# Performance work log

Hardware: AMD Instinct MI355X
Metric: run time of the kernel (lower is better)

Reference implementation:

```python
import jax, jax.numpy as jnp
import numpy as np

DIM = 256; Hh = 64; Ww = 64; L = Hh * Ww; B = 2
DIN = DIM          # expand = 1
DST = 16           # d_state
DTR = 16           # dt_rank = ceil(dim/16)
DCONV = 4


def _ln(x, g, b, eps=1e-5):
    m = jnp.mean(x, -1, keepdims=True)
    v = jnp.mean((x - m) ** 2, -1, keepdims=True)
    return (x - m) / jnp.sqrt(v + eps) * g + b


def _scan_dir(x, ep, z, convW, convb, xpW, dtW, dtb, A_log, Dp):
    # x, ep, z: (B, d_inner, L)
    xc = jnp.pad(x, ((0, 0), (0, 0), (DCONV - 1, 0)))  # causal depthwise conv
    xc = jax.lax.conv_general_dilated(
        xc, convW[:, None, :], (1,), 'VALID',
        feature_group_count=DIN, dimension_numbers=('NCH', 'OIH', 'NCH'))
    xs = jax.nn.silu(xc + convb[None, :, None])
    # cross: dt, B, C come from the OTHER modality's embedding (v7 cross-SSM)
    xdbl = jnp.einsum('bdl,kd->bkl', ep, xpW)               # (B, DTR+2N, L)
    dt = jax.nn.softplus(jnp.einsum('brl,dr->bdl', xdbl[:, :DTR], dtW) + dtb[None, :, None])
    Bm = xdbl[:, DTR:DTR + DST]                             # (B, N, L)
    Cm = xdbl[:, DTR + DST:]                                # (B, N, L)
    A = -jnp.exp(A_log)                                     # (d, N)
    dA = jnp.exp(jnp.einsum('bdl,dn->bdln', dt, A))         # (B, d, L, N)
    dBx = jnp.einsum('bdl,bnl,bdl->bdln', dt, Bm, xs)
    def comb(c1, c2):
        a1, b1 = c1; a2, b2 = c2
        return a1 * a2, a2 * b1 + b2
    _, h = jax.lax.associative_scan(comb, (dA, dBx), axis=2)  # h_l = dA_l h_{l-1} + dBx_l
    y = jnp.einsum('bdln,bnl->bdl', h, Cm) + Dp[None, :, None] * xs
    return y * jax.nn.silu(z)


def _mamba(u, e, in_proj_W, extra_proj_W,
           convf_W, convf_b, xprojf_W, dtf_W, dtf_b, A_log_f, D_f,
           convb_W, convb_b, xprojb_W, dtb_W, dtb_b, A_log_b, D_b,
           outnorm_g, outnorm_b, out_proj_W):
    xz = u @ in_proj_W.T                                    # (B, L, 2*d_inner)
    x = xz[..., :DIN].transpose(0, 2, 1)                    # (B, d, L)
    z = xz[..., DIN:].transpose(0, 2, 1)
    ep = (e @ extra_proj_W.T).transpose(0, 2, 1)            # (B, d, L)
    yf = _scan_dir(x, ep, z, convf_W, convf_b, xprojf_W, dtf_W, dtf_b, A_log_f, D_f)
    yb = jnp.flip(_scan_dir(jnp.flip(x, -1), jnp.flip(ep, -1), jnp.flip(z, -1),
                            convb_W, convb_b, xprojb_W, dtb_W, dtb_b, A_log_b, D_b), -1)
    y = (yf + yb) * 0.5                                     # if_devide_out
    y = _ln(y.transpose(0, 2, 1), outnorm_g, outnorm_b)     # use_norm
    return y @ out_proj_W.T


def setup_inputs() -> dict:
    key = jax.random.key(0)
    ks = jax.random.split(key, 20)
    s = 0.05
    dt_bias = float(np.log(np.expm1(0.01)))
    inp = {
        'input0': jax.random.normal(ks[0], (B, L, DIM), jnp.float32),
        'input1': jax.random.normal(ks[1], (B, L, DIM), jnp.float32),
        'norm0_g': jnp.ones((DIM,), jnp.float32), 'norm0_b': jnp.zeros((DIM,), jnp.float32),
        'norm1_g': jnp.ones((DIM,), jnp.float32), 'norm1_b': jnp.zeros((DIM,), jnp.float32),
        'cw_W': jax.random.normal(ks[2], (DIM, 2 * DIM), jnp.float32) * s,
        'cw_b': jnp.zeros((DIM,), jnp.float32),
        'in_proj_W': jax.random.normal(ks[3], (2 * DIN, DIM), jnp.float32) * s,
        'extra_proj_W': jax.random.normal(ks[4], (DIN, DIM), jnp.float32) * s,
        'convf_W': jax.random.normal(ks[5], (DIN, DCONV), jnp.float32) * 0.3,
        'convf_b': jnp.zeros((DIN,), jnp.float32),
        'xprojf_W': jax.random.normal(ks[6], (DTR + 2 * DST, DIN), jnp.float32) * s,
        'dtf_W': jax.random.normal(ks[7], (DIN, DTR), jnp.float32) * s,
        'dtf_b': jnp.full((DIN,), dt_bias, jnp.float32),
        'A_log_f': jnp.broadcast_to(jnp.log(jnp.arange(1, DST + 1, dtype=jnp.float32)), (DIN, DST)).copy(),
        'D_f': jnp.ones((DIN,), jnp.float32),
        'convb_W': jax.random.normal(ks[8], (DIN, DCONV), jnp.float32) * 0.3,
        'convb_b': jnp.zeros((DIN,), jnp.float32),
        'xprojb_W': jax.random.normal(ks[9], (DTR + 2 * DST, DIN), jnp.float32) * s,
        'dtb_W': jax.random.normal(ks[10], (DIN, DTR), jnp.float32) * s,
        'dtb_b': jnp.full((DIN,), dt_bias, jnp.float32),
        'A_log_b': jnp.broadcast_to(jnp.log(jnp.arange(1, DST + 1, dtype=jnp.float32)), (DIN, DST)).copy(),
        'D_b': jnp.ones((DIN,), jnp.float32),
        'outnorm_g': jnp.ones((DIN,), jnp.float32), 'outnorm_b': jnp.zeros((DIN,), jnp.float32),
        'out_proj_W': jax.random.normal(ks[11], (DIM, DIN), jnp.float32) * s,
        'post_g': jnp.ones((DIM,), jnp.float32), 'post_b': jnp.zeros((DIM,), jnp.float32),
    }
    return inp


def reference(input0, input1, norm0_g, norm0_b, norm1_g, norm1_b, cw_W, cw_b,
              in_proj_W, extra_proj_W,
              convf_W, convf_b, xprojf_W, dtf_W, dtf_b, A_log_f, D_f,
              convb_W, convb_b, xprojb_W, dtb_W, dtb_b, A_log_b, D_b,
              outnorm_g, outnorm_b, out_proj_W, post_g, post_b):
    skip = input0
    x0 = _ln(input0, norm0_g, norm0_b)
    x1 = _ln(input1, norm1_g, norm1_b)
    w = jax.nn.sigmoid(jnp.concatenate([x0, x1], -1) @ cw_W.T + cw_b)
    out = _mamba(x0, x1, in_proj_W, extra_proj_W,
                 convf_W, convf_b, xprojf_W, dtf_W, dtf_b, A_log_f, D_f,
                 convb_W, convb_b, xprojb_W, dtb_W, dtb_b, A_log_b, D_b,
                 outnorm_g, outnorm_b, out_proj_W)
    out = _ln(out, post_g, post_b)
    out = out * w + x0 * (1 - w)
    return out + skip
```

## Files before the change

### kernel.cpp

```cpp
#include <hip/hip_runtime.h>
#include <cstddef>

#define LL 4096
#define BB 2
#define DD 256
#define NEL ((size_t)BB * LL * DD)

typedef __bf16 bf16x8 __attribute__((ext_vector_type(8)));
typedef float f32x4 __attribute__((ext_vector_type(4)));
typedef unsigned short u16;

__device__ __forceinline__ float4 ld4(const float* p) { return *reinterpret_cast<const float4*>(p); }
__device__ __forceinline__ void st4(float* p, const float4 v) { *reinterpret_cast<float4*>(p) = v; }
__device__ __forceinline__ float softplusf(float x) { return fmaxf(x, 0.f) + log1pf(expf(-fabsf(x))); }
__device__ __forceinline__ u16 f2b(float f) {
    union { float f; unsigned u; } v; v.f = f;
    unsigned u = v.u;
    return (u16)((u + 0x7fffu + ((u >> 16) & 1u)) >> 16);
}

__device__ __forceinline__ void load16(const float* __restrict__ p, int fwd, float* dst) {
    if (fwd) {
#pragma unroll
        for (int k = 0; k < 4; ++k) {
            float4 v = ld4(p + 4 * k);
            dst[4 * k] = v.x; dst[4 * k + 1] = v.y; dst[4 * k + 2] = v.z; dst[4 * k + 3] = v.w;
        }
    } else {
#pragma unroll
        for (int k = 0; k < 4; ++k) {
            float4 v = ld4(p + 4 * k);
            dst[15 - 4 * k] = v.x; dst[14 - 4 * k] = v.y; dst[13 - 4 * k] = v.z; dst[12 - 4 * k] = v.w;
        }
    }
}


__global__ __launch_bounds__(256) void prep_q(
    const float* __restrict__ xpf, const float* __restrict__ xpb,
    const float* __restrict__ extW, float* __restrict__ Q, u16* __restrict__ wsH)
{
    const int r = blockIdx.x % 48;
    const int dir = blockIdx.x / 48;
    const int k = threadIdx.x;
    const float* xp = dir ? xpb : xpf;
    float s = 0.f;
    for (int n = 0; n < 256; ++n) s = fmaf(xp[r * 256 + n], extW[n * 256 + k], s);
    if (r < 16) Q[(dir * 16 + r) * 256 + k] = s;
    else        wsH[393216 + ((dir ? 32 : 0) + (r - 16)) * 256 + k] = f2b(s);
}

__global__ __launch_bounds__(256) void prep_w(
    const float* __restrict__ inW, const float* __restrict__ cwW,
    const float* __restrict__ outW, const float* __restrict__ dtfW,
    const float* __restrict__ dtbW, const float* __restrict__ Q,
    u16* __restrict__ wsH)
{
    const int idx = blockIdx.x * 256 + threadIdx.x;
    if (idx < 131072) {
        wsH[idx] = f2b(inW[idx]);
    } else if (idx < 262144) {
        wsH[idx] = f2b(cwW[idx - 131072]);
    } else if (idx < 393216) {
        const int i = idx - 262144;
        const int dir = i >> 16;
        const int j = i & 65535;
        const int n = j >> 8, k = j & 255;
        const float* dtW = dir ? dtbW : dtfW;
        const float* Qd = Q + dir * 4096;
        float s = 0.f;
#pragma unroll
        for (int r = 0; r < 16; ++r) s = fmaf(dtW[n * 16 + r], Qd[r * 256 + k], s);
        wsH[idx] = f2b(s);
    } else if (idx >= 409600 && idx < 475136) {
        wsH[idx] = f2b(outW[idx - 409600]);
    }
}

__global__ __launch_bounds__(64) void ln_rows(
    const float* __restrict__ in, float* __restrict__ outf, u16* __restrict__ outh,
    const float* __restrict__ g, const float* __restrict__ bb)
{
    const int row = blockIdx.x;
    const int t = threadIdx.x;
    const size_t off = (size_t)row * 256 + t * 4;
    float4 v = ld4(&in[off]);
    float s = v.x + v.y + v.z + v.w;
    float s2 = v.x * v.x + v.y * v.y + v.z * v.z + v.w * v.w;
#pragma unroll
    for (int dl = 1; dl < 64; dl <<= 1) { s += __shfl_xor(s, dl); s2 += __shfl_xor(s2, dl); }
    const float m = s * (1.f / 256.f);
    const float var = s2 * (1.f / 256.f) - m * m;
    const float rstd = rsqrtf(var + 1e-5f);
    const float4 gv = ld4(&g[t * 4]);
    const float4 bv = ld4(&bb[t * 4]);
    float4 r;
    r.x = (v.x - m) * rstd * gv.x + bv.x;
    r.y = (v.y - m) * rstd * gv.y + bv.y;
    r.z = (v.z - m) * rstd * gv.z + bv.z;
    r.w = (v.w - m) * rstd * gv.w + bv.w;
    if (outf) st4(&outf[off], r);
    ushort4 h; h.x = f2b(r.x); h.y = f2b(r.y); h.z = f2b(r.z); h.w = f2b(r.w);
    *reinterpret_cast<ushort4*>(&outh[off]) = h;
}

__global__ __launch_bounds__(256) void gemm_mfma(
    const u16* __restrict__ x0h, const u16* __restrict__ x1h, const u16* __restrict__ wsH,
    const float* __restrict__ cwb, const float* __restrict__ dtfb, const float* __restrict__ dtbb,
    float* __restrict__ xT, float* __restrict__ zT, float* __restrict__ wbuf,
    float* __restrict__ dtfT, float* __restrict__ dtbT,
    float* __restrict__ bcfT, float* __restrict__ bcbT)
{
    __shared__ __align__(16) u16 Blds[64 * 256];
    const int t = threadIdx.x;
    const int lane = t & 63;
    const int wid = t >> 6;
    const int col = lane & 15;
    const int kq = lane >> 4;
    const int m0 = blockIdx.x * 128;
    const int by = blockIdx.y;

    int seg, nbase, ldk, nhalf; const u16* W;
    if (by < 4)       { seg = 0; W = wsH + (size_t)(by * 64) * 256;                 ldk = 256; nhalf = 1; nbase = by * 64; }
    else if (by < 8)  { seg = 1; W = wsH + (size_t)(by * 64) * 256;                 ldk = 256; nhalf = 1; nbase = (by - 4) * 64; }
    else if (by < 12) { seg = 2; W = wsH + 131072 + (size_t)((by - 8) * 64) * 512;  ldk = 512; nhalf = 2; nbase = (by - 8) * 64; }
    else if (by < 16) { seg = 3; W = wsH + 262144 + (size_t)((by - 12) * 64) * 256; ldk = 256; nhalf = 1; nbase = (by - 12) * 64; }
    else if (by < 20) { seg = 4; W = wsH + 327680 + (size_t)((by - 16) * 64) * 256; ldk = 256; nhalf = 1; nbase = (by - 16) * 64; }
    else              { seg = 5; W = wsH + 393216;                                  ldk = 256; nhalf = 1; nbase = 0; }

    const u16* A0 = (seg >= 3) ? x1h : x0h;
    const int arow = m0 + wid * 32 + col;

    f32x4 acc[2][4] = {};
    for (int half = 0; half < nhalf; ++half) {
        if (half) __syncthreads();
#pragma unroll
        for (int it = 0; it < 8; ++it) {
            const int c = it * 256 + t;
            const int row = c >> 5, kc = c & 31;
            const bf16x8 v = *reinterpret_cast<const bf16x8*>(W + (size_t)row * ldk + half * 256 + kc * 8);
            const unsigned byt = ((unsigned)(row * 512 + kc * 16)) ^ (((unsigned)row & 7u) << 4);
            *reinterpret_cast<bf16x8*>(reinterpret_cast<char*>(Blds) + byt) = v;
        }
        __syncthreads();
        const u16* Ap = (seg == 2 && half) ? x1h : A0;
        const u16* Abase = Ap + (size_t)arow * 256;
        for (int k0 = 0; k0 < 256; k0 += 32) {
            const int kk = k0 + kq * 8;
            const bf16x8 a0 = *reinterpret_cast<const bf16x8*>(Abase + kk);
            const bf16x8 a1 = *reinterpret_cast<const bf16x8*>(Abase + 16 * 256 + kk);
#pragma unroll
            for (int nf = 0; nf < 4; ++nf) {
                const int n = nf * 16 + col;
                const unsigned byt = ((unsigned)(n * 512 + k0 * 2 + kq * 16)) ^ (((unsigned)n & 7u) << 4);
                const bf16x8 bfr = *reinterpret_cast<const bf16x8*>(reinterpret_cast<const char*>(Blds) + byt);
                acc[0][nf] = __builtin_amdgcn_mfma_f32_16x16x32_bf16(a0, bfr, acc[0][nf], 0, 0, 0);
                acc[1][nf] = __builtin_amdgcn_mfma_f32_16x16x32_bf16(a1, bfr, acc[1][nf], 0, 0, 0);
            }
        }
    }

    const int bb2 = m0 >> 12;
    const int l0 = m0 & (LL - 1);

    if (seg == 0 || seg == 1) {
        float* dst = (seg == 0) ? xT : zT;
#pragma unroll
        for (int rg = 0; rg < 2; ++rg) {
            const int mrow = wid * 32 + rg * 16 + kq * 4;
#pragma unroll
            for (int nf = 0; nf < 4; ++nf) {
                const int d = nbase + nf * 16 + col;
                *reinterpret_cast<f32x4*>(&dst[((size_t)bb2 * DD + d) * LL + l0 + mrow]) = acc[rg][nf];
            }
        }
    } else if (seg == 2) {
#pragma unroll
        for (int rg = 0; rg < 2; ++rg) {
            const int mrow = wid * 32 + rg * 16 + kq * 4;
#pragma unroll
            for (int nf = 0; nf < 4; ++nf) {
                const int n = nbase + nf * 16 + col;
                const float bv = cwb[n];
#pragma unroll
                for (int r = 0; r < 4; ++r)
                    wbuf[(size_t)(m0 + mrow + r) * 256 + n] = 1.f / (1.f + expf(-(acc[rg][nf][r] + bv)));
            }
        }
    } else if (seg == 3 || seg == 4) {
        const float* bias = (seg == 3) ? dtfb : dtbb;
        float* dst = (seg == 3) ? dtfT : dtbT;
#pragma unroll
        for (int rg = 0; rg < 2; ++rg) {
            const int mrow = wid * 32 + rg * 16 + kq * 4;
#pragma unroll
            for (int nf = 0; nf < 4; ++nf) {
                const int d = nbase + nf * 16 + col;
                const float bv = bias[d];
                f32x4 o;
#pragma unroll
                for (int r = 0; r < 4; ++r) o[r] = softplusf(acc[rg][nf][r] + bv);
                *reinterpret_cast<f32x4*>(&dst[((size_t)bb2 * DD + d) * LL + l0 + mrow]) = o;
            }
        }
    } else {
#pragma unroll
        for (int rg = 0; rg < 2; ++rg) {
            const int mrow = wid * 32 + rg * 16 + kq * 4;
#pragma unroll
            for (int nf = 0; nf < 4; ++nf) {
                const int n = nf * 16 + col;
                float* dst = (n < 32) ? bcfT : bcbT;
                const int comp = n & 31;
                *reinterpret_cast<f32x4*>(&dst[((size_t)bb2 * 32 + comp) * LL + l0 + mrow]) = acc[rg][nf];
            }
        }
    }
}

__global__ __launch_bounds__(256) void gemm_out_mfma(
    const u16* __restrict__ ynh, const u16* __restrict__ wsH, float* __restrict__ out)
{
    __shared__ __align__(16) u16 Blds[64 * 256];
    const int t = threadIdx.x;
    const int lane = t & 63;
    const int wid = t >> 6;
    const int col = lane & 15;
    const int kq = lane >> 4;
    const int m0 = blockIdx.x * 128;
    const int n0 = blockIdx.y * 64;
    const u16* W = wsH + 409600 + (size_t)n0 * 256;
    const int arow = m0 + wid * 32 + col;

#pragma unroll
    for (int it = 0; it < 8; ++it) {
        const int c = it * 256 + t;
        const int row = c >> 5, kc = c & 31;
        const bf16x8 v = *reinterpret_cast<const bf16x8*>(W + (size_t)row * 256 + kc * 8);
        const unsigned byt = ((unsigned)(row * 512 + kc * 16)) ^ (((unsigned)row & 7u) << 4);
        *reinterpret_cast<bf16x8*>(reinterpret_cast<char*>(Blds) + byt) = v;
    }
    __syncthreads();

    f32x4 acc[2][4] = {};
    const u16* Abase = ynh + (size_t)arow * 256;
    for (int k0 = 0; k0 < 256; k0 += 32) {
        const int kk = k0 + kq * 8;
        const bf16x8 a0 = *reinterpret_cast<const bf16x8*>(Abase + kk);
        const bf16x8 a1 = *reinterpret_cast<const bf16x8*>(Abase + 16 * 256 + kk);
#pragma unroll
        for (int nf = 0; nf < 4; ++nf) {
            const int n = nf * 16 + col;
            const unsigned byt = ((unsigned)(n * 512 + k0 * 2 + kq * 16)) ^ (((unsigned)n & 7u) << 4);
            const bf16x8 bfr = *reinterpret_cast<const bf16x8*>(reinterpret_cast<const char*>(Blds) + byt);
            acc[0][nf] = __builtin_amdgcn_mfma_f32_16x16x32_bf16(a0, bfr, acc[0][nf], 0, 0, 0);
            acc[1][nf] = __builtin_amdgcn_mfma_f32_16x16x32_bf16(a1, bfr, acc[1][nf], 0, 0, 0);
        }
    }
#pragma unroll
    for (int rg = 0; rg < 2; ++rg) {
        const int mrow = wid * 32 + rg * 16 + kq * 4;
#pragma unroll
        for (int nf = 0; nf < 4; ++nf) {
            const int n = n0 + nf * 16 + col;
#pragma unroll
            for (int r = 0; r < 4; ++r)
                out[(size_t)(m0 + mrow + r) * 256 + n] = acc[rg][nf][r];
        }
    }
}

__global__ __launch_bounds__(256) void scan_kernel(
    const float* __restrict__ xT, const float* __restrict__ zT,
    const float* __restrict__ dtfT, const float* __restrict__ dtbT,
    const float* __restrict__ bcfT, const float* __restrict__ bcbT,
    const float* __restrict__ cfW, const float* __restrict__ cfB,
    const float* __restrict__ cbW, const float* __restrict__ cbB,
    const float* __restrict__ AlF, const float* __restrict__ AlB,
    const float* __restrict__ DF, const float* __restrict__ DB,
    float* __restrict__ yF, float* __restrict__ yB)
{
    const int d = blockIdx.x;
    const int b = blockIdx.y;
    const int dir = blockIdx.z;
    const int t = threadIdx.x;
    const int lane = t & 63;
    const int wv = t >> 6;
    const int fwd = (dir == 0);
    const float* dtT = fwd ? dtfT : dtbT;
    const float* bcT = fwd ? bcfT : bcbT;
    const float* cW  = fwd ? cfW  : cbW;
    const float* cBv = fwd ? cfB  : cbB;
    const float* Al  = fwd ? AlF  : AlB;
    const float* Dp  = fwd ? DF   : DB;
    float* yout = fwd ? yF : yB;

    const int p0 = t * 16;
    const size_t xbase = ((size_t)b * DD + d) * LL;
    const int ls = LL - 16 - p0;
    const int off16 = fwd ? p0 : ls;

    const float Dd = Dp[d];
    const float c0 = cW[d * 4 + 0], c1 = cW[d * 4 + 1], c2 = cW[d * 4 + 2], c3 = cW[d * 4 + 3];
    const float cbias = cBv[d];

    float xq[19];
    if (fwd) {
#pragma unroll
        for (int k = 0; k < 4; ++k) {
            float4 v = ld4(&xT[xbase + p0 + 4 * k]);
            xq[3 + 4 * k] = v.x; xq[4 + 4 * k] = v.y; xq[5 + 4 * k] = v.z; xq[6 + 4 * k] = v.w;
        }
        xq[2] = (p0 >= 1) ? xT[xbase + p0 - 1] : 0.f;
        xq[1] = (p0 >= 2) ? xT[xbase + p0 - 2] : 0.f;
        xq[0] = (p0 >= 3) ? xT[xbase + p0 - 3] : 0.f;
    } else {
#pragma unroll
        for (int k = 0; k < 4; ++k) {
            float4 v = ld4(&xT[xbase + ls + 4 * k]);
            xq[18 - 4 * k] = v.x; xq[17 - 4 * k] = v.y; xq[16 - 4 * k] = v.z; xq[15 - 4 * k] = v.w;
        }
        xq[2] = (p0 >= 1) ? xT[xbase + LL - p0] : 0.f;
        xq[1] = (p0 >= 2) ? xT[xbase + LL + 1 - p0] : 0.f;
        xq[0] = (p0 >= 3) ? xT[xbase + LL + 2 - p0] : 0.f;
    }

    float dt[16];
    load16(&dtT[xbase + off16], fwd, dt);

    float dtxs[16], yacc[16];
#pragma unroll
    for (int s = 0; s < 16; ++s) {
        float c = fmaf(xq[s], c0, fmaf(xq[s + 1], c1, fmaf(xq[s + 2], c2, fmaf(xq[s + 3], c3, cbias))));
        const float xv = c / (1.f + expf(-c));
        dtxs[s] = dt[s] * xv;
        yacc[s] = Dd * xv;
    }

    const float* bcb0 = bcT + (size_t)b * 32 * LL + off16;

    __shared__ float wPs[2][4];
    __shared__ float wSs[2][4];

#pragma unroll 1
    for (int n = 0; n < 16; ++n) {
        const float a2 = -expf(Al[d * 16 + n]) * 1.4426950408889634f;
        float Bn[16];
        load16(bcb0 + (size_t)n * LL, fwd, Bn);
        float pw[16], hl[16];
        float Pl = 1.f, Sl = 0.f;
#pragma unroll
        for (int s = 0; s < 16; ++s) {
            const float w = exp2f(dt[s] * a2);
            Sl = fmaf(w, Sl, dtxs[s] * Bn[s]);
            Pl *= w;
            pw[s] = Pl; hl[s] = Sl;
        }
        float Cn[16];
        load16(bcb0 + (size_t)(16 + n) * LL, fwd, Cn);
#pragma unroll
        for (int dl = 1; dl < 64; dl <<= 1) {
            const float Pp = __shfl_up(Pl, dl);
            const float Sp = __shfl_up(Sl, dl);
            if (lane >= dl) { Sl = fmaf(Pl, Sp, Sl); Pl *= Pp; }
        }
        const int buf = n & 1;
        if (lane == 63) { wPs[buf][wv] = Pl; wSs[buf][wv] = Sl; }
        __syncthreads();
        float WSv = 0.f;
#pragma unroll
        for (int w2 = 0; w2 < 3; ++w2)
            if (w2 < wv) WSv = fmaf(wPs[buf][w2], WSv, wSs[buf][w2]);
        const float Pex = __shfl_up(Pl, 1);
        const float Sex = __shfl_up(Sl, 1);
        const float hin = lane ? fmaf(Pex, WSv, Sex) : WSv;
#pragma unroll
        for (int s = 0; s < 16; ++s)
            yacc[s] = fmaf(fmaf(pw[s], hin, hl[s]), Cn[s], yacc[s]);
    }

    float zq[16];
    load16(&zT[xbase + off16], fwd, zq);
    float yv[16];
#pragma unroll
    for (int s = 0; s < 16; ++s) {
        const float zz = zq[s];
        yv[s] = yacc[s] * zz / (1.f + expf(-zz));
    }

    if (fwd) {
#pragma unroll
        for (int k = 0; k < 4; ++k)
            st4(&yout[xbase + p0 + 4 * k], make_float4(yv[4 * k], yv[4 * k + 1], yv[4 * k + 2], yv[4 * k + 3]));
    } else {
#pragma unroll
        for (int k = 0; k < 4; ++k)
            st4(&yout[xbase + ls + 4 * k], make_float4(yv[15 - 4 * k], yv[14 - 4 * k], yv[13 - 4 * k], yv[12 - 4 * k]));
    }
}

__global__ __launch_bounds__(256) void comb_ln(
    const float* __restrict__ yF, const float* __restrict__ yB,
    const float* __restrict__ g, const float* __restrict__ bb,
    u16* __restrict__ out)
{
    __shared__ float tile[256][33];
    __shared__ float rs[8][32];
    __shared__ float rs2[8][32];
    const int b = blockIdx.y;
    const int l0 = blockIdx.x * 32;
    const int t = threadIdx.x;
    {
        const size_t base = ((size_t)b * DD + t) * LL + l0;
#pragma unroll
        for (int k = 0; k < 8; ++k) {
            float4 f = ld4(&yF[base + 4 * k]);
            float4 bv = ld4(&yB[base + 4 * k]);
            tile[t][4 * k + 0] = (f.x + bv.x) * 0.5f;
            tile[t][4 * k + 1] = (f.y + bv.y) * 0.5f;
            tile[t][4 * k + 2] = (f.z + bv.z) * 0.5f;
            tile[t][4 * k + 3] = (f.w + bv.w) * 0.5f;
        }
    }
    __syncthreads();
    const int l = t & 31;
    const int grp = t >> 5;
    float s = 0.f, s2 = 0.f;
#pragma unroll
    for (int i = 0; i < 32; ++i) {
        const float v = tile[grp * 32 + i][l];
        s += v; s2 = fmaf(v, v, s2);
    }
    rs[grp][l] = s; rs2[grp][l] = s2;
    __syncthreads();
    float st = 0.f, st2 = 0.f;
#pragma unroll
    for (int gq = 0; gq < 8; ++gq) { st += rs[gq][l]; st2 += rs2[gq][l]; }
    const float m = st * (1.f / 256.f);
    const float var = st2 * (1.f / 256.f) - m * m;
    const float rstd = rsqrtf(var + 1e-5f);
    const size_t obase = ((size_t)b * LL + l0 + l) * 256 + grp * 32;
#pragma unroll
    for (int k = 0; k < 8; ++k) {
        const float4 gv = ld4(&g[grp * 32 + 4 * k]);
        const float4 bv2 = ld4(&bb[grp * 32 + 4 * k]);
        ushort4 h;
        h.x = f2b((tile[grp * 32 + 4 * k + 0][l] - m) * rstd * gv.x + bv2.x);
        h.y = f2b((tile[grp * 32 + 4 * k + 1][l] - m) * rstd * gv.y + bv2.y);
        h.z = f2b((tile[grp * 32 + 4 * k + 2][l] - m) * rstd * gv.z + bv2.z);
        h.w = f2b((tile[grp * 32 + 4 * k + 3][l] - m) * rstd * gv.w + bv2.w);
        *reinterpret_cast<ushort4*>(&out[obase + 4 * k]) = h;
    }
}

__global__ __launch_bounds__(64) void final_kernel(
    const float* __restrict__ o, const float* __restrict__ w,
    const float* __restrict__ x0n, const float* __restrict__ in0,
    const float* __restrict__ pg, const float* __restrict__ pb,
    float* __restrict__ outp)
{
    const int row = blockIdx.x;
    const int t = threadIdx.x;
    const size_t off = (size_t)row * 256 + t * 4;
    float4 v = ld4(&o[off]);
    float s = v.x + v.y + v.z + v.w;
    float s2 = v.x * v.x + v.y * v.y + v.z * v.z + v.w * v.w;
#pragma unroll
    for (int dl = 1; dl < 64; dl <<= 1) { s += __shfl_xor(s, dl); s2 += __shfl_xor(s2, dl); }
    const float m = s * (1.f / 256.f);
    const float var = s2 * (1.f / 256.f) - m * m;
    const float rstd = rsqrtf(var + 1e-5f);
    const float4 gv = ld4(&pg[t * 4]);
    const float4 bv = ld4(&pb[t * 4]);
    const float4 wv = ld4(&w[off]);
    const float4 xv = ld4(&x0n[off]);
    const float4 iv = ld4(&in0[off]);
    float4 r;
    r.x = ((v.x - m) * rstd * gv.x + bv.x) * wv.x + xv.x * (1.f - wv.x) + iv.x;
    r.y = ((v.y - m) * rstd * gv.y + bv.y) * wv.y + xv.y * (1.f - wv.y) + iv.y;
    r.z = ((v.z - m) * rstd * gv.z + bv.z) * wv.z + xv.z * (1.f - wv.z) + iv.z;
    r.w = ((v.w - m) * rstd * gv.w + bv.w) * wv.w + xv.w * (1.f - wv.w) + iv.w;
    st4(&outp[off], r);
}

extern "C" void kernel_launch(void* const* d_in, const int* in_sizes, int n_in,
                              void* d_out, int out_size, void* d_ws, size_t ws_size,
                              hipStream_t stream) {
    (void)in_sizes; (void)n_in; (void)out_size; (void)ws_size;
    const float* in0      = (const float*)d_in[0];
    const float* in1      = (const float*)d_in[1];
    const float* norm0_g  = (const float*)d_in[2];
    const float* norm0_b  = (const float*)d_in[3];
    const float* norm1_g  = (const float*)d_in[4];
    const float* norm1_b  = (const float*)d_in[5];
    const float* cw_W     = (const float*)d_in[6];
    const float* cw_b     = (const float*)d_in[7];
    const float* in_proj_W    = (const float*)d_in[8];
    const float* extra_proj_W = (const float*)d_in[9];
    const float* convf_W  = (const float*)d_in[10];
    const float* convf_b  = (const float*)d_in[11];
    const float* xprojf_W = (const float*)d_in[12];
    const float* dtf_W    = (const float*)d_in[13];
    const float* dtf_b    = (const float*)d_in[14];
    const float* A_log_f  = (const float*)d_in[15];
    const float* D_f      = (const float*)d_in[16];
    const float* convb_W  = (const float*)d_in[17];
    const float* convb_b  = (const float*)d_in[18];
    const float* xprojb_W = (const float*)d_in[19];
    const float* dtb_W    = (const float*)d_in[20];
    const float* dtb_b    = (const float*)d_in[21];
    const float* A_log_b  = (const float*)d_in[22];
    const float* D_b      = (const float*)d_in[23];
    const float* outnorm_g = (const float*)d_in[24];
    const float* outnorm_b = (const float*)d_in[25];
    const float* out_proj_W = (const float*)d_in[26];
    const float* post_g   = (const float*)d_in[27];
    const float* post_b   = (const float*)d_in[28];

    float* ws = (float*)d_ws;
    float* x0n   = ws;
    float* xT    = ws + NEL;
    float* zT    = ws + 2 * NEL;
    float* dtfT  = ws + 3 * NEL;
    float* dtbT  = ws + 4 * NEL;
    float* wbuf  = ws + 5 * NEL;
    float* yF    = ws + 6 * NEL;
    float* yB    = ws + 7 * NEL;
    float* bcfT  = ws + 8 * NEL;
    float* bcbT  = bcfT + (size_t)BB * 32 * LL;
    u16*   wsH   = (u16*)(bcbT + (size_t)BB * 32 * LL);
    float* Qtmp  = (float*)(wsH + 475136);

    u16* x0h = (u16*)yF;
    u16* x1h = x0h + NEL;
    u16* ynormh = (u16*)dtfT;
    float* obuf = dtbT;

    prep_q<<<96, 256, 0, stream>>>(xprojf_W, xprojb_W, extra_proj_W, Qtmp, wsH);
    prep_w<<<1856, 256, 0, stream>>>(in_proj_W, cw_W, out_proj_W, dtf_W, dtb_W, Qtmp, wsH);
    ln_rows<<<BB * LL, 64, 0, stream>>>(in0, x0n, x0h, norm0_g, norm0_b);
    ln_rows<<<BB * LL, 64, 0, stream>>>(in1, nullptr, x1h, norm1_g, norm1_b);
    gemm_mfma<<<dim3(64, 21, 1), 256, 0, stream>>>(x0h, x1h, wsH, cw_b, dtf_b, dtb_b,
                                                   xT, zT, wbuf, dtfT, dtbT, bcfT, bcbT);
    scan_kernel<<<dim3(256, 2, 2), 256, 0, stream>>>(xT, zT, dtfT, dtbT, bcfT, bcbT,
                                                     convf_W, convf_b, convb_W, convb_b,
                                                     A_log_f, A_log_b, D_f, D_b,
                                                     yF, yB);
    comb_ln<<<dim3(128, 2, 1), 256, 0, stream>>>(yF, yB, outnorm_g, outnorm_b, ynormh);
    gemm_out_mfma<<<dim3(64, 4, 1), 256, 0, stream>>>(ynormh, wsH, obuf);
    final_kernel<<<BB * LL, 64, 0, stream>>>(obuf, wbuf, x0n, in0, post_g, post_b, (float*)d_out);
}
```

Baseline: 132.7 us.

## Split scan state dimension across two blocks and store partial outputs as bf16

The scan kernel now launches twice as many blocks, with each block handling 8 of the 16 state channels and writing a partial output. The D*x term is added only in one half, and both partials are multiplied by silu(z). Partials are stored as bf16 and summed in comb_ln, which now reads four bf16 buffers. This is meant to add parallelism to the scan and cut output bytes. In exchange the conv, silu and z work is done twice, and rounding each partial to bf16 adds error.

```diff
diff --git a/kernel.cpp b/kernel.cpp
--- a/kernel.cpp
+++ b/kernel.cpp
@@ -17,6 +17,9 @@
     union { float f; unsigned u; } v; v.f = f;
     unsigned u = v.u;
     return (u16)((u + 0x7fffu + ((u >> 16) & 1u)) >> 16);
+}
+__device__ __forceinline__ float b2f(unsigned bits16) {
+    union { unsigned u; float f; } v; v.u = bits16 << 16; return v.f;
 }
 
 __device__ __forceinline__ void load16(const float* __restrict__ p, int fwd, float* dst) {
@@ -278,11 +281,12 @@
     const float* __restrict__ cbW, const float* __restrict__ cbB,
     const float* __restrict__ AlF, const float* __restrict__ AlB,
     const float* __restrict__ DF, const float* __restrict__ DB,
-    float* __restrict__ yF, float* __restrict__ yB)
+    u16* __restrict__ yFh, u16* __restrict__ yBh)
 {
     const int d = blockIdx.x;
     const int b = blockIdx.y;
-    const int dir = blockIdx.z;
+    const int dir = blockIdx.z >> 1;
+    const int half = blockIdx.z & 1;
     const int t = threadIdx.x;
     const int lane = t & 63;
     const int wv = t >> 6;
@@ -293,7 +297,7 @@
     const float* cBv = fwd ? cfB  : cbB;
     const float* Al  = fwd ? AlF  : AlB;
     const float* Dp  = fwd ? DF   : DB;
-    float* yout = fwd ? yF : yB;
+    u16* yout = (fwd ? yFh : yBh) + (size_t)half * NEL;
 
     const int p0 = t * 16;
     const size_t xbase = ((size_t)b * DD + d) * LL;
@@ -334,7 +338,7 @@
         float c = fmaf(xq[s], c0, fmaf(xq[s + 1], c1, fmaf(xq[s + 2], c2, fmaf(xq[s + 3], c3, cbias))));
         const float xv = c / (1.f + expf(-c));
         dtxs[s] = dt[s] * xv;
-        yacc[s] = Dd * xv;
+        yacc[s] = half ? (Dd * xv) : 0.f;
     }
 
     const float* bcb0 = bcT + (size_t)b * 32 * LL + off16;
@@ -343,10 +347,11 @@
     __shared__ float wSs[2][4];
 
 #pragma unroll 1
-    for (int n = 0; n < 16; ++n) {
-        const float a2 = -expf(Al[d * 16 + n]) * 1.4426950408889634f;
+    for (int n = 0; n < 8; ++n) {
+        const int ng = half * 8 + n;
+        const float a2 = -expf(Al[d * 16 + ng]) * 1.4426950408889634f;
         float Bn[16];
-        load16(bcb0 + (size_t)n * LL, fwd, Bn);
+        load16(bcb0 + (size_t)ng * LL, fwd, Bn);
         float pw[16], hl[16];
         float Pl = 1.f, Sl = 0.f;
 #pragma unroll
@@ -357,7 +362,7 @@
             pw[s] = Pl; hl[s] = Sl;
         }
         float Cn[16];
-        load16(bcb0 + (size_t)(16 + n) * LL, fwd, Cn);
+        load16(bcb0 + (size_t)(16 + ng) * LL, fwd, Cn);
 #pragma unroll
         for (int dl = 1; dl < 64; dl <<= 1) {
             const float Pp = __shfl_up(Pl, dl);
@@ -388,19 +393,26 @@
         yv[s] = yacc[s] * zz / (1.f + expf(-zz));
     }
 
-    if (fwd) {
-#pragma unroll
-        for (int k = 0; k < 4; ++k)
-            st4(&yout[xbase + p0 + 4 * k], make_float4(yv[4 * k], yv[4 * k + 1], yv[4 * k + 2], yv[4 * k + 3]));
-    } else {
-#pragma unroll
-        for (int k = 0; k < 4; ++k)
-            st4(&yout[xbase + ls + 4 * k], make_float4(yv[15 - 4 * k], yv[14 - 4 * k], yv[13 - 4 * k], yv[12 - 4 * k]));
+#pragma unroll
+    for (int g = 0; g < 2; ++g) {
+        uint4 U;
+        unsigned* up = reinterpret_cast<unsigned*>(&U);
+        if (fwd) {
+#pragma unroll
+            for (int j = 0; j < 4; ++j)
+                up[j] = (unsigned)f2b(yv[8 * g + 2 * j]) | ((unsigned)f2b(yv[8 * g + 2 * j + 1]) << 16);
+            *reinterpret_cast<uint4*>(&yout[xbase + p0 + 8 * g]) = U;
+        } else {
+#pragma unroll
+            for (int j = 0; j < 4; ++j)
+                up[j] = (unsigned)f2b(yv[15 - 8 * g - 2 * j]) | ((unsigned)f2b(yv[15 - 8 * g - 2 * j - 1]) << 16);
+            *reinterpret_cast<uint4*>(&yout[xbase + ls + 8 * g]) = U;
+        }
     }
 }
 
 __global__ __launch_bounds__(256) void comb_ln(
-    const float* __restrict__ yF, const float* __restrict__ yB,
+    const u16* __restrict__ yFh, const u16* __restrict__ yBh,
     const float* __restrict__ g, const float* __restrict__ bb,
     u16* __restrict__ out)
 {
@@ -411,15 +423,30 @@
     const int l0 = blockIdx.x * 32;
     const int t = threadIdx.x;
     {
-        const size_t base = ((size_t)b * DD + t) * LL + l0;
-#pragma unroll
-        for (int k = 0; k < 8; ++k) {
-            float4 f = ld4(&yF[base + 4 * k]);
-            float4 bv = ld4(&yB[base + 4 * k]);
-            tile[t][4 * k + 0] = (f.x + bv.x) * 0.5f;
-            tile[t][4 * k + 1] = (f.y + bv.y) * 0.5f;
-            tile[t][4 * k + 2] = (f.z + bv.z) * 0.5f;
-            tile[t][4 * k + 3] = (f.w + bv.w) * 0.5f;
+        const size_t rowoff = ((size_t)b * DD + t) * LL + l0;
+        const u16* s0 = yFh + rowoff;
+        const u16* s1 = yFh + NEL + rowoff;
+        const u16* s2 = yBh + rowoff;
+        const u16* s3 = yBh + NEL + rowoff;
+#pragma unroll
+        for (int k = 0; k < 4; ++k) {
+            const uint4 a = *reinterpret_cast<const uint4*>(s0 + 8 * k);
+            const uint4 c = *reinterpret_cast<const uint4*>(s1 + 8 * k);
+            const uint4 e = *reinterpret_cast<const uint4*>(s2 + 8 * k);
+            const uint4 f = *reinterpret_cast<const uint4*>(s3 + 8 * k);
+            const unsigned* au = reinterpret_cast<const unsigned*>(&a);
+            const unsigned* cu = reinterpret_cast<const unsigned*>(&c);
+            const unsigned* eu = reinterpret_cast<const unsigned*>(&e);
+            const unsigned* fu = reinterpret_cast<const unsigned*>(&f);
+#pragma unroll
+            for (int j = 0; j < 4; ++j) {
+                const float lo = b2f(au[j] & 0xffffu) + b2f(cu[j] & 0xffffu)
+                               + b2f(eu[j] & 0xffffu) + b2f(fu[j] & 0xffffu);
+                const float hi = b2f(au[j] >> 16) + b2f(cu[j] >> 16)
+                               + b2f(eu[j] >> 16) + b2f(fu[j] >> 16);
+                tile[t][8 * k + 2 * j]     = lo * 0.5f;
+                tile[t][8 * k + 2 * j + 1] = hi * 0.5f;
+            }
         }
     }
     __syncthreads();
@@ -533,6 +560,8 @@
 
     u16* x0h = (u16*)yF;
     u16* x1h = x0h + NEL;
+    u16* yFh = (u16*)yF;
+    u16* yBh = (u16*)yB;
     u16* ynormh = (u16*)dtfT;
     float* obuf = dtbT;
 
@@ -542,11 +571,11 @@
     ln_rows<<<BB * LL, 64, 0, stream>>>(in1, nullptr, x1h, norm1_g, norm1_b);
     gemm_mfma<<<dim3(64, 21, 1), 256, 0, stream>>>(x0h, x1h, wsH, cw_b, dtf_b, dtb_b,
                                                    xT, zT, wbuf, dtfT, dtbT, bcfT, bcbT);
-    scan_kernel<<<dim3(256, 2, 2), 256, 0, stream>>>(xT, zT, dtfT, dtbT, bcfT, bcbT,
+    scan_kernel<<<dim3(256, 2, 4), 256, 0, stream>>>(xT, zT, dtfT, dtbT, bcfT, bcbT,
                                                      convf_W, convf_b, convb_W, convb_b,
                                                      A_log_f, A_log_b, D_f, D_b,
-                                                     yF, yB);
-    comb_ln<<<dim3(128, 2, 1), 256, 0, stream>>>(yF, yB, outnorm_g, outnorm_b, ynormh);
+                                                     yFh, yBh);
+    comb_ln<<<dim3(128, 2, 1), 256, 0, stream>>>(yFh, yBh, outnorm_g, outnorm_b, ynormh);
     gemm_out_mfma<<<dim3(64, 4, 1), 256, 0, stream>>>(ynormh, wsH, obuf);
     final_kernel<<<BB * LL, 64, 0, stream>>>(obuf, wbuf, x0n, in0, post_g, post_b, (float*)d_out);
 }
```

Measured after the change: 138.6 us. +4.4%, slower.
